# Kernel optimization log

Measured on AMD Instinct MI355X. Metric: run time of the kernel, lower is better.

The kernel has to match this reference:

```python
import jax, jax.numpy as jnp
import numpy as np
from jax import lax

DN = ('NCHW', 'OIHW', 'NCHW')

def conv(x, w, b, stride=1):
    y = lax.conv_general_dilated(x, w, window_strides=(stride, stride),
                                 padding='VALID', dimension_numbers=DN)
    return y + b[None, :, None, None]

def maxpool(x, k=3, s=2):
    return lax.reduce_window(x, -jnp.inf, lax.max,
                             (1, 1, k, k), (1, 1, s, s), 'VALID')

def setup_inputs() -> dict:
    key = jax.random.key(0)
    ks = jax.random.split(key, 7)
    B = 2048
    x = jax.random.normal(ks[0], (B, 1, 28, 28), dtype=jnp.float32)
    w1 = jax.random.normal(ks[1], (64, 1, 3, 3), dtype=jnp.float32)
    b1 = jax.random.normal(ks[2], (64,), dtype=jnp.float32)
    w2 = jax.random.normal(ks[3], (64, 64, 3, 3), dtype=jnp.float32)
    b2 = jax.random.normal(ks[4], (64,), dtype=jnp.float32)
    w3 = jax.random.normal(ks[5], (10, 64, 4, 4), dtype=jnp.float32)
    b3 = jax.random.normal(ks[6], (10,), dtype=jnp.float32)
    return {"x": x, "w1": w1, "b1": b1, "w2": w2, "b2": b2, "w3": w3, "b3": b3}

def reference(x, w1, b1, w2, b2, w3, b3):
    h = conv(x, w1, b1)            # [B,64,26,26]
    h = maxpool(h)                 # [B,64,12,12]
    h = jnp.maximum(h, 0.0)
    h = conv(h, w2, b2)            # [B,64,10,10]
    h = maxpool(h)                 # [B,64,4,4]
    h = jnp.maximum(h, 0.0)
    h = conv(h, w3, b3)            # [B,10,1,1]
    return h.reshape(h.shape[0], -1)  # [B,10]
```

## Files before the change

### kernel.cpp

```cpp
#include <hip/hip_runtime.h>


typedef __attribute__((ext_vector_type(8))) short short8;
typedef __attribute__((ext_vector_type(4))) float f32x4;

__device__ inline short f2bf(float f) {
    union { float f; unsigned u; } v; v.f = f;
    unsigned r = (v.u + 0x7FFFu + ((v.u >> 16) & 1u)) >> 16;
    return (short)r;
}
__device__ inline float bf2f(short s) {
    union { unsigned u; float f; } v; v.u = ((unsigned)(unsigned short)s) << 16;
    return v.f;
}

__global__ __launch_bounds__(256) void prep_w2(const float* __restrict__ w2,
                                               short* __restrict__ w2r) {
    int i = blockIdx.x * 256 + threadIdx.x;
    if (i >= 36864) return;
    int s = i >> 12, cout = (i >> 6) & 63, cin = i & 63;
    w2r[i] = f2bf(w2[cout * 576 + cin * 9 + s]);
}

__global__ __launch_bounds__(256) void convnet_fused(
    const float* __restrict__ x,
    const float* __restrict__ w1,
    const float* __restrict__ b1,
    const short* __restrict__ w2r,
    const float* __restrict__ b2,
    const float* __restrict__ w3,
    const float* __restrict__ b3,
    float* __restrict__ out)
{
    __shared__ float lds_f[5968];
    short* h1t   = (short*)lds_f;
    float* img   = lds_f + 5184;
    short* cbuf  = (short*)lds_f;
    float* h2t   = lds_f + 3232;
    float* prt   = lds_f;

    const int n_img = blockIdx.x;
    const int t = threadIdx.x;
    const int c = t >> 2;
    const int q = t & 3;

    const float* img_g = x + (size_t)n_img * 784;
    for (int i = t; i < 784; i += 256) img[i] = img_g[i];
    __syncthreads();

    {
        const int oy = (q >> 1) * 6, ox = (q & 1) * 6;
        const int iy0 = 2 * oy, ix0 = 2 * ox;
        float w[9];
        #pragma unroll
        for (int k = 0; k < 9; ++k) w[k] = w1[c * 9 + k];
        const float bias = b1[c];

        float in0[15], in1[15], in2[15];
        #pragma unroll
        for (int s = 0; s < 15; ++s) in0[s] = img[(iy0 + 0) * 28 + ix0 + s];
        #pragma unroll
        for (int s = 0; s < 15; ++s) in1[s] = img[(iy0 + 1) * 28 + ix0 + s];
        float cm[3][6];

        #pragma unroll
        for (int r = 0; r < 13; ++r) {
            #pragma unroll
            for (int s = 0; s < 15; ++s) in2[s] = img[(iy0 + r + 2) * 28 + ix0 + s];
            #pragma unroll
            for (int px = 0; px < 6; ++px) cm[r % 3][px] = -1e30f;
            #pragma unroll
            for (int xx = 0; xx < 13; ++xx) {
                float a = bias;
                #pragma unroll
                for (int j = 0; j < 3; ++j) {
                    a += in0[xx + j] * w[j];
                    a += in1[xx + j] * w[3 + j];
                    a += in2[xx + j] * w[6 + j];
                }
                if ((xx & 1) == 0) {
                    if (xx >= 2 && xx <= 12) cm[r % 3][xx / 2 - 1] = fmaxf(cm[r % 3][xx / 2 - 1], a);
                    if (xx <= 10)            cm[r % 3][xx / 2]     = fmaxf(cm[r % 3][xx / 2], a);
                } else {
                    cm[r % 3][xx / 2] = fmaxf(cm[r % 3][xx / 2], a);
                }
            }
            if (r >= 2 && (r & 1) == 0) {
                const int py = r / 2 - 1;
                #pragma unroll
                for (int px = 0; px < 6; ++px) {
                    float m = fmaxf(fmaxf(cm[0][px], cm[1][px]), cm[2][px]);
                    h1t[((oy + py) * 12 + ox + px) * 72 + c] = f2bf(fmaxf(m, 0.0f));
                }
            }
            #pragma unroll
            for (int s = 0; s < 15; ++s) { in0[s] = in1[s]; in1[s] = in2[s]; }
        }
    }
    __syncthreads();

    const int wv = t >> 6, lane = t & 63;
    const int quad = lane >> 4, mrow = lane & 15;
    {
        int base_el[7];
        #pragma unroll
        for (int nt = 0; nt < 7; ++nt) {
            int n = nt * 16 + mrow; if (n > 99) n = 99;
            int y = n / 10, xx = n - y * 10;
            base_el[nt] = (y * 12 + xx) * 72;
        }
        f32x4 acc[7];
        #pragma unroll
        for (int nt = 0; nt < 7; ++nt) acc[nt] = (f32x4){0.f, 0.f, 0.f, 0.f};

        #pragma unroll
        for (int ks = 0; ks < 18; ++ks) {
            const int s = ks >> 1, h = ks & 1;
            const int ky = s / 3, kx = s - ky * 3;
            const short8 a = *(const short8*)(w2r + s * 4096 + (wv * 16 + mrow) * 64
                                              + h * 32 + quad * 8);
            #pragma unroll
            for (int nt = 0; nt < 7; ++nt) {
                const short8 b = *(const short8*)(h1t + base_el[nt]
                                                  + (ky * 12 + kx) * 72 + h * 32 + quad * 8);
                acc[nt] = __builtin_amdgcn_mfma_f32_16x16x32_bf16(a, b, acc[nt], 0, 0, 0);
            }
        }
        __syncthreads();
        #pragma unroll
        for (int nt = 0; nt < 7; ++nt) {
            const int n = nt * 16 + mrow;
            if (n < 100) {
                #pragma unroll
                for (int r = 0; r < 4; ++r) {
                    const int cout = wv * 16 + quad * 4 + r;
                    cbuf[cout * 101 + n] = f2bf(acc[nt][r] + b2[cout]);
                }
            }
        }
    }
    __syncthreads();

    {
        const short* cb = cbuf + c * 101;
        #pragma unroll
        for (int k = 0; k < 4; ++k) {
            const int pos = q * 4 + k;
            const int py = pos >> 2, px = pos & 3;
            float m = -1e30f;
            #pragma unroll
            for (int a = 0; a < 3; ++a)
                #pragma unroll
                for (int b = 0; b < 3; ++b)
                    m = fmaxf(m, bf2f(cb[(2 * py + a) * 10 + (2 * px + b)]));
            h2t[pos * 65 + c] = fmaxf(m, 0.0f);
        }
    }
    __syncthreads();

    if (t < 160) {
        const int o = t >> 4, l = t & 15;
        const float* w3o = w3 + o * 1024;
        float s = 0.0f;
        #pragma unroll
        for (int cc = 0; cc < 4; ++cc) {
            const int cin = l * 4 + cc;
            const float4 wv4a = *(const float4*)(w3o + cin * 16);
            const float4 wv4b = *(const float4*)(w3o + cin * 16 + 4);
            const float4 wv4c = *(const float4*)(w3o + cin * 16 + 8);
            const float4 wv4d = *(const float4*)(w3o + cin * 16 + 12);
            const float* hh = h2t + cin;
            s += hh[0*65] * wv4a.x + hh[1*65] * wv4a.y + hh[2*65] * wv4a.z + hh[3*65] * wv4a.w;
            s += hh[4*65] * wv4b.x + hh[5*65] * wv4b.y + hh[6*65] * wv4b.z + hh[7*65] * wv4b.w;
            s += hh[8*65] * wv4c.x + hh[9*65] * wv4c.y + hh[10*65] * wv4c.z + hh[11*65] * wv4c.w;
            s += hh[12*65] * wv4d.x + hh[13*65] * wv4d.y + hh[14*65] * wv4d.z + hh[15*65] * wv4d.w;
        }
        prt[t] = s;
    }
    __syncthreads();
    if (t < 10) {
        float s = b3[t];
        #pragma unroll
        for (int l = 0; l < 16; ++l) s += prt[t * 16 + l];
        out[(size_t)n_img * 10 + t] = s;
    }
}

extern "C" void kernel_launch(void* const* d_in, const int* in_sizes, int n_in,
                              void* d_out, int out_size, void* d_ws, size_t ws_size,
                              hipStream_t stream) {
    const float* x  = (const float*)d_in[0];
    const float* w1 = (const float*)d_in[1];
    const float* b1 = (const float*)d_in[2];
    const float* w2 = (const float*)d_in[3];
    const float* b2 = (const float*)d_in[4];
    const float* w3 = (const float*)d_in[5];
    const float* b3 = (const float*)d_in[6];
    float* out = (float*)d_out;
    short* w2r = (short*)d_ws;

    const int B = in_sizes[0] / 784;
    prep_w2<<<144, 256, 0, stream>>>(w2, w2r);
    convnet_fused<<<B, 256, 0, stream>>>(x, w1, b1, w2r, b2, w3, b3, out);
}
```

Measured before the change: 115.2 us.

## Shrink LDS footprint with bf16 image and XOR-swizzled h1 layout

Stores the input image in LDS as bf16 instead of fp32 and replaces the padded stride-72 h1 layout with an unpadded stride-64 layout using an XOR swizzle to avoid bank conflicts. This cuts LDS per block (5968 to 5000 floats) and adds a launch-bounds min-blocks hint of 8 to raise occupancy. The price is rounding the input image to bf16 before conv1, which adds error, and the extra address arithmetic for the swizzle and unpacking.

```diff
diff --git a/kernel.cpp b/kernel.cpp
--- a/kernel.cpp
+++ b/kernel.cpp
@@ -22,7 +22,7 @@
     w2r[i] = f2bf(w2[cout * 576 + cin * 9 + s]);
 }
 
-__global__ __launch_bounds__(256) void convnet_fused(
+__global__ __launch_bounds__(256, 8) void convnet_fused(
     const float* __restrict__ x,
     const float* __restrict__ w1,
     const float* __restrict__ b1,
@@ -32,9 +32,9 @@
     const float* __restrict__ b3,
     float* __restrict__ out)
 {
-    __shared__ float lds_f[5968];
+    __shared__ float lds_f[5000];
     short* h1t   = (short*)lds_f;
-    float* img   = lds_f + 5184;
+    short* imgbf = (short*)(lds_f + 4608);
     short* cbuf  = (short*)lds_f;
     float* h2t   = lds_f + 3232;
     float* prt   = lds_f;
@@ -45,7 +45,7 @@
     const int q = t & 3;
 
     const float* img_g = x + (size_t)n_img * 784;
-    for (int i = t; i < 784; i += 256) img[i] = img_g[i];
+    for (int i = t; i < 784; i += 256) imgbf[i] = f2bf(img_g[i]);
     __syncthreads();
 
     {
@@ -57,16 +57,25 @@
         const float bias = b1[c];
 
         float in0[15], in1[15], in2[15];
-        #pragma unroll
-        for (int s = 0; s < 15; ++s) in0[s] = img[(iy0 + 0) * 28 + ix0 + s];
-        #pragma unroll
-        for (int s = 0; s < 15; ++s) in1[s] = img[(iy0 + 1) * 28 + ix0 + s];
+
+        #define LOADROW(dst, row) do { \
+            const unsigned* p32 = (const unsigned*)(imgbf + (row) * 28 + ix0); \
+            _Pragma("unroll") \
+            for (int d = 0; d < 8; ++d) { \
+                const unsigned u = p32[d]; \
+                union { unsigned u; float f; } lo, hi; \
+                lo.u = u << 16; hi.u = u & 0xFFFF0000u; \
+                if (2 * d < 15) (dst)[2 * d] = lo.f; \
+                if (2 * d + 1 < 15) (dst)[2 * d + 1] = hi.f; \
+            } } while (0)
+
+        LOADROW(in0, iy0 + 0);
+        LOADROW(in1, iy0 + 1);
         float cm[3][6];
 
         #pragma unroll
         for (int r = 0; r < 13; ++r) {
-            #pragma unroll
-            for (int s = 0; s < 15; ++s) in2[s] = img[(iy0 + r + 2) * 28 + ix0 + s];
+            LOADROW(in2, iy0 + r + 2);
             #pragma unroll
             for (int px = 0; px < 6; ++px) cm[r % 3][px] = -1e30f;
             #pragma unroll
@@ -90,24 +99,26 @@
                 #pragma unroll
                 for (int px = 0; px < 6; ++px) {
                     float m = fmaxf(fmaxf(cm[0][px], cm[1][px]), cm[2][px]);
-                    h1t[((oy + py) * 12 + ox + px) * 72 + c] = f2bf(fmaxf(m, 0.0f));
+                    const int pos = (oy + py) * 12 + ox + px;
+                    h1t[pos * 64 + (c ^ ((pos & 7) << 3))] = f2bf(fmaxf(m, 0.0f));
                 }
             }
             #pragma unroll
             for (int s = 0; s < 15; ++s) { in0[s] = in1[s]; in1[s] = in2[s]; }
         }
+        #undef LOADROW
     }
     __syncthreads();
 
     const int wv = t >> 6, lane = t & 63;
     const int quad = lane >> 4, mrow = lane & 15;
     {
-        int base_el[7];
+        int pos_b[7];
         #pragma unroll
         for (int nt = 0; nt < 7; ++nt) {
             int n = nt * 16 + mrow; if (n > 99) n = 99;
             int y = n / 10, xx = n - y * 10;
-            base_el[nt] = (y * 12 + xx) * 72;
+            pos_b[nt] = y * 12 + xx;
         }
         f32x4 acc[7];
         #pragma unroll
@@ -117,12 +128,15 @@
         for (int ks = 0; ks < 18; ++ks) {
             const int s = ks >> 1, h = ks & 1;
             const int ky = s / 3, kx = s - ky * 3;
+            const int koff = ky * 12 + kx;
+            const int hoff = h * 32 + quad * 8;
             const short8 a = *(const short8*)(w2r + s * 4096 + (wv * 16 + mrow) * 64
                                               + h * 32 + quad * 8);
             #pragma unroll
             for (int nt = 0; nt < 7; ++nt) {
-                const short8 b = *(const short8*)(h1t + base_el[nt]
-                                                  + (ky * 12 + kx) * 72 + h * 32 + quad * 8);
+                const int pos = pos_b[nt] + koff;
+                const short8 b = *(const short8*)(h1t + pos * 64
+                                                  + (hoff ^ ((pos & 7) << 3)));
                 acc[nt] = __builtin_amdgcn_mfma_f32_16x16x32_bf16(a, b, acc[nt], 0, 0, 0);
             }
         }
```

Result: slower. 185.7 us (+61.2%).
